# Kernel optimization log

Hardware: AMD Instinct MI355X
Metric: run time of the kernel (lower is better)

## Reference

```python
import jax, jax.numpy as jnp
import numpy as np

HEADS = 4
HID = 64
IN_DIM = 128
N_WIRES, N_TERM, N_ACT = 50, 20, 10
NEG_SLOPE = 0.2


def gat_conv(x, src, dst, ea, W, We, a_src, a_dst, a_edge, bias, concat):
    """PyG GATConv with edge features, add_self_loops=True, fill_value='mean'."""
    N = x.shape[0]
    H, F = a_src.shape
    # --- add self loops; self-loop edge_attr = mean of incoming edge_attr ---
    deg = jax.ops.segment_sum(jnp.ones((ea.shape[0],), x.dtype), dst, num_segments=N)
    loop_attr = jax.ops.segment_sum(ea, dst, num_segments=N) / jnp.maximum(deg, 1.0)[:, None]
    ar = jnp.arange(N)
    src = jnp.concatenate([src, ar])
    dst = jnp.concatenate([dst, ar])
    ea = jnp.concatenate([ea, loop_attr], axis=0)
    # --- linear transforms ---
    h = (x @ W).reshape(N, H, F)                      # [N,H,F]
    a_s = jnp.einsum('nhf,hf->nh', h, a_src)          # [N,H]
    a_d = jnp.einsum('nhf,hf->nh', h, a_dst)
    he = (ea @ We).reshape(-1, H, F)                  # [E2,H,F]
    a_e = jnp.einsum('ehf,hf->eh', he, a_edge)        # [E2,H]
    # --- attention logits + softmax over edges grouped by destination ---
    alpha = jax.nn.leaky_relu(a_s[src] + a_d[dst] + a_e, negative_slope=NEG_SLOPE)
    amax = jax.ops.segment_max(alpha, dst, num_segments=N)
    ex = jnp.exp(alpha - amax[dst])
    denom = jax.ops.segment_sum(ex, dst, num_segments=N)
    alpha = ex / (denom[dst] + 1e-16)                 # [E2,H]
    # --- message passing: gather src feats, weight, scatter-sum to dst ---
    out = jax.ops.segment_sum(h[src] * alpha[..., None], dst, num_segments=N)  # [N,H,F]
    out = out.reshape(N, H * F) if concat else out.mean(axis=1)
    return out + bias


def setup_inputs() -> dict:
    key = jax.random.key(0)
    ks = jax.random.split(key, 24)
    N, E = 20000, 320000
    x = jax.random.normal(ks[0], (N, IN_DIM), jnp.float32)
    edge_index = jax.random.randint(ks[1], (2, E), 0, N, dtype=jnp.int64)
    edge_attr = jax.random.normal(ks[2], (E, 2), jnp.float32)
    s = 0.1
    p = {
        'W1': jax.random.normal(ks[3], (IN_DIM, HEADS * HID)) * s,
        'We1': jax.random.normal(ks[4], (2, HEADS * HID)) * s,
        'as1': jax.random.normal(ks[5], (HEADS, HID)) * s,
        'ad1': jax.random.normal(ks[6], (HEADS, HID)) * s,
        'ae1': jax.random.normal(ks[7], (HEADS, HID)) * s,
        'b1': jnp.zeros((HEADS * HID,), jnp.float32),
        'W2': jax.random.normal(ks[8], (HEADS * HID, HEADS * HID)) * s,
        'We2': jax.random.normal(ks[9], (2, HEADS * HID)) * s,
        'as2': jax.random.normal(ks[10], (HEADS, HID)) * s,
        'ad2': jax.random.normal(ks[11], (HEADS, HID)) * s,
        'ae2': jax.random.normal(ks[12], (HEADS, HID)) * s,
        'b2': jnp.zeros((HID,), jnp.float32),
        'Ww': jax.random.normal(ks[13], (HID, N_WIRES)) * s,
        'bw': jnp.zeros((N_WIRES,), jnp.float32),
        'Wt': jax.random.normal(ks[14], (HID, N_TERM)) * s,
        'bt': jnp.zeros((N_TERM,), jnp.float32),
        'Wa': jax.random.normal(ks[15], (HID, N_ACT)) * s,
        'ba': jnp.zeros((N_ACT,), jnp.float32),
    }
    return {'x': x, 'edge_index': edge_index, 'edge_attr': edge_attr, **p}


def reference(x, edge_index, edge_attr, W1, We1, as1, ad1, ae1, b1,
              W2, We2, as2, ad2, ae2, b2, Ww, bw, Wt, bt, Wa, ba):
    src, dst = edge_index[0], edge_index[1]
    h = jax.nn.elu(gat_conv(x, src, dst, edge_attr, W1, We1, as1, ad1, ae1, b1, True))
    h = jax.nn.elu(gat_conv(h, src, dst, edge_attr, W2, We2, as2, ad2, ae2, b2, False))
    wire_logits = h @ Ww + bw
    terminal_logits = h @ Wt + bt
    action_logits = h @ Wa + ba
    return (wire_logits, terminal_logits, action_logits)
```

## Files before the change

### kernel.cpp

```cpp
#include <hip/hip_runtime.h>
#include <math.h>

#define N_NODES 20000
#define N_EDGES 320000
#define D1      256
#define WCAP    128
#define NSCAT   1250

typedef __attribute__((ext_vector_type(8))) short    bf16x8;
typedef __attribute__((ext_vector_type(4))) float    f32x4;
typedef __attribute__((ext_vector_type(8))) unsigned short u16x8;

__device__ inline float wred_sum(float v) {
#pragma unroll
  for (int o = 32; o > 0; o >>= 1) v += __shfl_xor(v, o, 64);
  return v;
}

__device__ inline unsigned short f2b(float v) {
  unsigned u = __float_as_uint(v);
  unsigned r = (u + 0x7fffu + ((u >> 16) & 1u)) >> 16;
  return (unsigned short)r;
}
__device__ inline float b2f(unsigned short h) {
  return __uint_as_float(((unsigned)h) << 16);
}

__global__ __launch_bounds__(256) void k_prep(
    const int* __restrict__ ei, const float* __restrict__ ea,
    int* __restrict__ deg, int* __restrict__ src_slot, float* __restrict__ ea_slot,
    const float* __restrict__ W1, unsigned short* __restrict__ WT1h,
    unsigned short* __restrict__ WT1l,
    const float* __restrict__ W2, unsigned short* __restrict__ WT2h,
    unsigned short* __restrict__ WT2l,
    const float* __restrict__ We1, const float* __restrict__ ae1,
    const float* __restrict__ We2, const float* __restrict__ ae2,
    float* __restrict__ qb,
    const float* __restrict__ Ww, const float* __restrict__ Wt,
    const float* __restrict__ Wa,
    const float* __restrict__ bw, const float* __restrict__ bt,
    const float* __restrict__ ba,
    unsigned short* __restrict__ WallTh, unsigned short* __restrict__ WallTl,
    float* __restrict__ biasAll) {
  int bid = blockIdx.x, t = threadIdx.x;
  if (bid < NSCAT) {
    int e = bid * 256 + t;
    int s = ei[e], d = ei[N_EDGES + e];
    float2 e2 = *(const float2*)&ea[e * 2];
    int pos = atomicAdd(&deg[d], 1);
    if (pos < WCAP) {
      int slot = d * WCAP + pos;
      src_slot[slot] = s;
      *(float2*)&ea_slot[(size_t)slot * 2] = e2;
    }
  } else if (bid < NSCAT + 128) {
    int i = (bid - NSCAT) * 256 + t;
    int k = i >> 8, n = i & 255;
    float v = W1[i];
    unsigned short h = f2b(v);
    WT1h[n * 128 + k] = h;
    WT1l[n * 128 + k] = f2b(v - b2f(h));
  } else if (bid < NSCAT + 384) {
    int i = (bid - NSCAT - 128) * 256 + t;
    int k = i >> 8, n = i & 255;
    float v = W2[i];
    unsigned short h = f2b(v);
    WT2h[n * 256 + k] = h;
    WT2l[n * 256 + k] = f2b(v - b2f(h));
  } else if (bid == NSCAT + 384) {
    int lane = t & 63, w = t >> 6;
    const float* We = (w >> 1) ? We2 : We1;
    const float* ae = (w >> 1) ? ae2 : ae1;
    int c = w & 1;
#pragma unroll
    for (int h = 0; h < 4; h++) {
      float p = We[c * D1 + h * 64 + lane] * ae[h * 64 + lane];
      p = wred_sum(p);
      if (lane == 0) qb[(w >> 1) * 8 + c * 4 + h] = p;
    }
    if (t < 80) biasAll[t] = (t < 50) ? bw[t] : (t < 70) ? bt[t - 50] : ba[t - 70];
  } else {
    int i = (bid - NSCAT - 385) * 256 + t;
    int j = i >> 6, f = i & 63;
    float v = 0.f;
    if (j < 50)      v = Ww[f * 50 + j];
    else if (j < 70) v = Wt[f * 20 + (j - 50)];
    else if (j < 80) v = Wa[f * 10 + (j - 70)];
    unsigned short h = f2b(v);
    WallTh[j * 64 + f] = h;
    WallTl[j * 64 + f] = f2b(v - b2f(h));
  }
}

#define LDK 40
template <bool AF32>
__global__ __launch_bounds__(256) void k_gemm_mfma(
    const float* __restrict__ Af, const unsigned short* __restrict__ Ah,
    const unsigned short* __restrict__ BTh, const unsigned short* __restrict__ BTl,
    unsigned short* __restrict__ Chi,
    const float* __restrict__ asw, const float* __restrict__ adw,
    float* __restrict__ asb, float* __restrict__ adb,
    int M, int K) {
  __shared__ unsigned short sAh[128 * LDK];
  __shared__ unsigned short sBh[128 * LDK], sBl[128 * LDK];
  int tid = threadIdx.x;
  int lane = tid & 63, wid = tid >> 6;
  int wr = wid >> 1, wc = wid & 1;
  int row0 = blockIdx.y * 128, col0 = blockIdx.x * 128;
  int aRow = wr * 64, bRow = wc * 64;

  f32x4 acc[4][4];
#pragma unroll
  for (int i = 0; i < 4; i++)
#pragma unroll
    for (int j = 0; j < 4; j++) acc[i][j] = (f32x4){0.f, 0.f, 0.f, 0.f};

  int c0i = tid * 2;
  int r0 = c0i >> 2, ko0 = (c0i & 3) * 8;
  int c1i = tid * 2 + 1;
  int r1 = c1i >> 2, ko1 = (c1i & 3) * 8;

  int q8 = (lane >> 4) * 8;
  int rsel = lane & 15;

  const u16x8 z8 = {0, 0, 0, 0, 0, 0, 0, 0};
  int ga0 = row0 + r0, ga1 = row0 + r1;
  bool va0 = ga0 < M, va1 = ga1 < M;
  size_t arow0 = (size_t)ga0 * K, arow1 = (size_t)ga1 * K;
  size_t brow0 = (size_t)(col0 + r0) * K, brow1 = (size_t)(col0 + r1) * K;

  auto ldA = [&](size_t rowoff, bool valid, int kk) -> u16x8 {
    if (!valid) return z8;
    if constexpr (AF32) {
      float4 f0 = *(const float4*)&Af[rowoff + kk];
      float4 f1 = *(const float4*)&Af[rowoff + kk + 4];
      u16x8 r;
      r[0] = f2b(f0.x); r[1] = f2b(f0.y); r[2] = f2b(f0.z); r[3] = f2b(f0.w);
      r[4] = f2b(f1.x); r[5] = f2b(f1.y); r[6] = f2b(f1.z); r[7] = f2b(f1.w);
      return r;
    } else {
      return *(const u16x8*)&Ah[rowoff + kk];
    }
  };

  u16x8 ca0 = ldA(arow0, va0, ko0), ca1 = ldA(arow1, va1, ko1);
  u16x8 cbh0 = *(const u16x8*)&BTh[brow0 + ko0];
  u16x8 cbl0 = *(const u16x8*)&BTl[brow0 + ko0];
  u16x8 cbh1 = *(const u16x8*)&BTh[brow1 + ko1];
  u16x8 cbl1 = *(const u16x8*)&BTl[brow1 + ko1];

  for (int k0 = 0; k0 < K; k0 += 32) {
    *(u16x8*)&sAh[r0 * LDK + ko0] = ca0;
    *(u16x8*)&sAh[r1 * LDK + ko1] = ca1;
    *(u16x8*)&sBh[r0 * LDK + ko0] = cbh0;
    *(u16x8*)&sBl[r0 * LDK + ko0] = cbl0;
    *(u16x8*)&sBh[r1 * LDK + ko1] = cbh1;
    *(u16x8*)&sBl[r1 * LDK + ko1] = cbl1;
    __syncthreads();

    if (k0 + 32 < K) {
      int kn = k0 + 32;
      ca0 = ldA(arow0, va0, kn + ko0);
      ca1 = ldA(arow1, va1, kn + ko1);
      cbh0 = *(const u16x8*)&BTh[brow0 + kn + ko0];
      cbl0 = *(const u16x8*)&BTl[brow0 + kn + ko0];
      cbh1 = *(const u16x8*)&BTh[brow1 + kn + ko1];
      cbl1 = *(const u16x8*)&BTl[brow1 + kn + ko1];
    }

    bf16x8 fah[4], fbh[4], fbl[4];
#pragma unroll
    for (int i = 0; i < 4; i++) {
      int ar = aRow + i * 16 + rsel;
      int br = bRow + i * 16 + rsel;
      fah[i] = *(const bf16x8*)&sAh[ar * LDK + q8];
      fbh[i] = *(const bf16x8*)&sBh[br * LDK + q8];
      fbl[i] = *(const bf16x8*)&sBl[br * LDK + q8];
    }
#pragma unroll
    for (int i = 0; i < 4; i++)
#pragma unroll
      for (int j = 0; j < 4; j++) {
        acc[i][j] = __builtin_amdgcn_mfma_f32_16x16x32_bf16(fah[i], fbh[j], acc[i][j], 0, 0, 0);
        acc[i][j] = __builtin_amdgcn_mfma_f32_16x16x32_bf16(fah[i], fbl[j], acc[i][j], 0, 0, 0);
      }
    __syncthreads();
  }

  int rq = (lane >> 4) * 4;
  int head = (col0 + bRow) >> 6;
  float sa[4], sd[4];
#pragma unroll
  for (int j = 0; j < 4; j++) {
    sa[j] = asw[head * 64 + j * 16 + rsel];
    sd[j] = adw[head * 64 + j * 16 + rsel];
  }
#pragma unroll
  for (int i = 0; i < 4; i++) {
#pragma unroll
    for (int j = 0; j < 4; j++) {
      int gcol = col0 + bRow + j * 16 + rsel;
#pragma unroll
      for (int r = 0; r < 4; r++) {
        int grow = row0 + aRow + i * 16 + rq + r;
        if (grow < M) Chi[(size_t)grow * D1 + gcol] = f2b(acc[i][j][r]);
      }
    }
#pragma unroll
    for (int r = 0; r < 4; r++) {
      float ps = 0.f, pd = 0.f;
#pragma unroll
      for (int j = 0; j < 4; j++) {
        ps = fmaf(acc[i][j][r], sa[j], ps);
        pd = fmaf(acc[i][j][r], sd[j], pd);
      }
#pragma unroll
      for (int o = 1; o < 16; o <<= 1) {
        ps += __shfl_xor(ps, o, 64);
        pd += __shfl_xor(pd, o, 64);
      }
      int grow = row0 + aRow + i * 16 + rq + r;
      if ((lane & 15) == 0 && grow < M) {
        asb[grow * 4 + head] = ps;
        adb[grow * 4 + head] = pd;
      }
    }
  }
}

__global__ __launch_bounds__(256) void k_heads_mfma(
    const unsigned short* __restrict__ Ah, const unsigned short* __restrict__ Al,
    const unsigned short* __restrict__ BTh, const unsigned short* __restrict__ BTl,
    const float* __restrict__ biasAll, float* __restrict__ out, int M) {
  __shared__ unsigned short sAh[128 * LDK], sAl[128 * LDK];
  __shared__ unsigned short sBh[128 * LDK], sBl[128 * LDK];
  const int K = 64;
  int tid = threadIdx.x;
  int lane = tid & 63, wid = tid >> 6;
  int wr = wid >> 1, wc = wid & 1;
  int row0 = blockIdx.x * 128;
  int aRow = wr * 64, bRow = wc * 64;

  f32x4 acc[4][4];
#pragma unroll
  for (int i = 0; i < 4; i++)
#pragma unroll
    for (int j = 0; j < 4; j++) acc[i][j] = (f32x4){0.f, 0.f, 0.f, 0.f};

  int c0i = tid * 2;
  int r0 = c0i >> 2, ko0 = (c0i & 3) * 8;
  int c1i = tid * 2 + 1;
  int r1 = c1i >> 2, ko1 = (c1i & 3) * 8;
  int q8 = (lane >> 4) * 8;
  int rsel = lane & 15;

  for (int k0 = 0; k0 < K; k0 += 32) {
    u16x8 z = {0, 0, 0, 0, 0, 0, 0, 0};
    int ga0 = row0 + r0, ga1 = row0 + r1;
    u16x8 vah0 = (ga0 < M) ? *(const u16x8*)&Ah[(size_t)ga0 * K + k0 + ko0] : z;
    u16x8 val0 = (ga0 < M) ? *(const u16x8*)&Al[(size_t)ga0 * K + k0 + ko0] : z;
    u16x8 vah1 = (ga1 < M) ? *(const u16x8*)&Ah[(size_t)ga1 * K + k0 + ko1] : z;
    u16x8 val1 = (ga1 < M) ? *(const u16x8*)&Al[(size_t)ga1 * K + k0 + ko1] : z;
    u16x8 vbh0 = *(const u16x8*)&BTh[(size_t)r0 * K + k0 + ko0];
    u16x8 vbl0 = *(const u16x8*)&BTl[(size_t)r0 * K + k0 + ko0];
    u16x8 vbh1 = *(const u16x8*)&BTh[(size_t)r1 * K + k0 + ko1];
    u16x8 vbl1 = *(const u16x8*)&BTl[(size_t)r1 * K + k0 + ko1];
    *(u16x8*)&sAh[r0 * LDK + ko0] = vah0;
    *(u16x8*)&sAl[r0 * LDK + ko0] = val0;
    *(u16x8*)&sAh[r1 * LDK + ko1] = vah1;
    *(u16x8*)&sAl[r1 * LDK + ko1] = val1;
    *(u16x8*)&sBh[r0 * LDK + ko0] = vbh0;
    *(u16x8*)&sBl[r0 * LDK + ko0] = vbl0;
    *(u16x8*)&sBh[r1 * LDK + ko1] = vbh1;
    *(u16x8*)&sBl[r1 * LDK + ko1] = vbl1;
    __syncthreads();

    bf16x8 fah[4], fal[4], fbh[4], fbl[4];
#pragma unroll
    for (int i = 0; i < 4; i++) {
      int ar = aRow + i * 16 + rsel;
      int br = bRow + i * 16 + rsel;
      fah[i] = *(const bf16x8*)&sAh[ar * LDK + q8];
      fal[i] = *(const bf16x8*)&sAl[ar * LDK + q8];
      fbh[i] = *(const bf16x8*)&sBh[br * LDK + q8];
      fbl[i] = *(const bf16x8*)&sBl[br * LDK + q8];
    }
#pragma unroll
    for (int i = 0; i < 4; i++)
#pragma unroll
      for (int j = 0; j < 4; j++) {
        acc[i][j] = __builtin_amdgcn_mfma_f32_16x16x32_bf16(fah[i], fbh[j], acc[i][j], 0, 0, 0);
        acc[i][j] = __builtin_amdgcn_mfma_f32_16x16x32_bf16(fah[i], fbl[j], acc[i][j], 0, 0, 0);
        acc[i][j] = __builtin_amdgcn_mfma_f32_16x16x32_bf16(fal[i], fbh[j], acc[i][j], 0, 0, 0);
      }
    __syncthreads();
  }

  int rq = (lane >> 4) * 4;
#pragma unroll
  for (int j = 0; j < 4; j++) {
    int gcol = bRow + j * 16 + rsel;
    if (gcol < 80) {
      float bj = biasAll[gcol];
      float* op; int cols, jj;
      if (gcol < 50)      { op = out;                 cols = 50; jj = gcol; }
      else if (gcol < 70) { op = out + N_NODES * 50;  cols = 20; jj = gcol - 50; }
      else                { op = out + N_NODES * 70;  cols = 10; jj = gcol - 70; }
#pragma unroll
      for (int i = 0; i < 4; i++) {
#pragma unroll
        for (int r = 0; r < 4; r++) {
          int grow = row0 + aRow + i * 16 + rq + r;
          if (grow < M) op[(size_t)grow * cols + jj] = acc[i][j][r] + bj;
        }
      }
    }
  }
}

template <bool CONCAT>
__global__ __launch_bounds__(256) void k_aggregate(
    const unsigned short* __restrict__ feath,
    const int* __restrict__ deg_arr,
    const int* __restrict__ src_slot, const float* __restrict__ ea_slot,
    const float* __restrict__ asb, const float* __restrict__ adb,
    const float* __restrict__ q, const float* __restrict__ bias,
    unsigned short* __restrict__ outh,
    unsigned short* __restrict__ outf_h, unsigned short* __restrict__ outf_l) {
  __shared__ float slog[4][4][WCAP];
  __shared__ int   ssrc[4][WCAP];
  int t = threadIdx.x, lane = t & 63, w = t >> 6;
  int n = blockIdx.x * 4 + w;
  int deg = min(deg_arr[n], WCAP);
  int b = n * WCAP;

  float4 qv0 = *(const float4*)q;
  float4 qv1 = *(const float4*)(q + 4);
  float4 ad4 = *(const float4*)&adb[(size_t)n * 4];
  float4 asn = *(const float4*)&asb[(size_t)n * 4];

  int degR = (deg + 15) & ~15;
  if (degR == 0) degR = 16;
  int   sreg[2] = {n, n};
  float e0r[2] = {0.f, 0.f}, e1r[2] = {0.f, 0.f};
#pragma unroll
  for (int p = 0; p < 2; p++) {
    int j = lane + p * 64;
    if (j < degR) {
      int s = n; float e0v = 0.f, e1v = 0.f;
      if (j < deg) {
        s = src_slot[b + j];
        float2 ee = *(const float2*)&ea_slot[(size_t)(b + j) * 2];
        e0v = ee.x; e1v = ee.y;
      }
      ssrc[w][j] = s;
      sreg[p] = s; e0r[p] = e0v; e1r[p] = e1v;
    }
  }
  int es = lane >> 5, cg = lane & 31, hh = cg >> 3;
  const unsigned short* fb = feath + cg * 8;
  u16x8 pf[8];
#pragma unroll
  for (int q8 = 0; q8 < 8; q8++) {
    int s = __shfl(sreg[0], 2 * q8 + es, 64);
    pf[q8] = *(const u16x8*)&fb[(size_t)s * D1];
  }
  float lv[2][4];
#pragma unroll
  for (int p = 0; p < 2; p++) {
    int j = lane + p * 64;
    float l0 = -1e30f, l1 = -1e30f, l2 = -1e30f, l3 = -1e30f;
    if (j < deg) {
      float4 as4 = *(const float4*)&asb[(size_t)sreg[p] * 4];
      float e0v = e0r[p], e1v = e1r[p];
      l0 = as4.x + ad4.x + e0v * qv0.x + e1v * qv1.x; l0 = (l0 > 0.f) ? l0 : 0.2f * l0;
      l1 = as4.y + ad4.y + e0v * qv0.y + e1v * qv1.y; l1 = (l1 > 0.f) ? l1 : 0.2f * l1;
      l2 = as4.z + ad4.z + e0v * qv0.z + e1v * qv1.z; l2 = (l2 > 0.f) ? l2 : 0.2f * l2;
      l3 = as4.w + ad4.w + e0v * qv0.w + e1v * qv1.w; l3 = (l3 > 0.f) ? l3 : 0.2f * l3;
    }
    lv[p][0] = l0; lv[p][1] = l1; lv[p][2] = l2; lv[p][3] = l3;
  }
  float dinv = 1.f / fmaxf((float)deg, 1.f);
  float e0m = wred_sum(e0r[0] + e0r[1]) * dinv;
  float e1m = wred_sum(e1r[0] + e1r[1]) * dinv;
  float ls[4];
  ls[0] = asn.x + ad4.x + e0m * qv0.x + e1m * qv1.x;
  ls[1] = asn.y + ad4.y + e0m * qv0.y + e1m * qv1.y;
  ls[2] = asn.z + ad4.z + e0m * qv0.z + e1m * qv1.z;
  ls[3] = asn.w + ad4.w + e0m * qv0.w + e1m * qv1.w;
#pragma unroll
  for (int h = 0; h < 4; h++) ls[h] = (ls[h] > 0.f) ? ls[h] : 0.2f * ls[h];
  float ex[2][4];
#pragma unroll
  for (int p = 0; p < 2; p++)
#pragma unroll
    for (int h = 0; h < 4; h++) ex[p][h] = __expf(lv[p][h]);
  float inv[4], wself[4];
#pragma unroll
  for (int h = 0; h < 4; h++) {
    float eself = __expf(ls[h]);
    float ss = wred_sum(ex[0][h] + ex[1][h]) + eself;
    inv[h] = 1.f / (ss + 1e-16f);
    wself[h] = eself * inv[h];
  }
#pragma unroll
  for (int p = 0; p < 2; p++) {
    int j = lane + p * 64;
    if (j < degR) {
#pragma unroll
      for (int h = 0; h < 4; h++) slog[w][h][j] = ex[p][h] * inv[h];
    }
  }
  float acc8[8] = {};
#pragma unroll
  for (int q8 = 0; q8 < 8; q8++) {
    float ww = slog[w][hh][2 * q8 + es];
#pragma unroll
    for (int k = 0; k < 8; k++) acc8[k] = fmaf(ww, b2f((unsigned short)pf[q8][k]), acc8[k]);
  }
  for (int j0 = 16; j0 < degR; j0 += 16) {
    u16x8 f[8];
#pragma unroll
    for (int q8 = 0; q8 < 8; q8++)
      f[q8] = *(const u16x8*)&fb[(size_t)ssrc[w][j0 + 2 * q8 + es] * D1];
#pragma unroll
    for (int q8 = 0; q8 < 8; q8++) {
      float ww = slog[w][hh][j0 + 2 * q8 + es];
#pragma unroll
      for (int k = 0; k < 8; k++) acc8[k] = fmaf(ww, b2f((unsigned short)f[q8][k]), acc8[k]);
    }
  }
  if (es == 0) {
    u16x8 fs = *(const u16x8*)&fb[(size_t)n * D1];
    float ws2 = wself[hh];
#pragma unroll
    for (int k = 0; k < 8; k++) acc8[k] = fmaf(ws2, b2f((unsigned short)fs[k]), acc8[k]);
  }
#pragma unroll
  for (int k = 0; k < 8; k++) acc8[k] += __shfl_xor(acc8[k], 32, 64);
  if (CONCAT) {
    if (es == 0) {
      u16x8 hi8;
#pragma unroll
      for (int k = 0; k < 8; k++) {
        float v2 = acc8[k] + bias[cg * 8 + k];
        v2 = (v2 > 0.f) ? v2 : (__expf(v2) - 1.f);
        hi8[k] = f2b(v2);
      }
      *(u16x8*)&outh[(size_t)n * D1 + cg * 8] = hi8;
    }
  } else {
#pragma unroll
    for (int k = 0; k < 8; k++) {
      acc8[k] += __shfl_xor(acc8[k], 8, 64);
      acc8[k] += __shfl_xor(acc8[k], 16, 64);
    }
    if (es == 0 && cg < 8) {
      u16x8 hi8, lo8;
#pragma unroll
      for (int k = 0; k < 8; k++) {
        float v2 = acc8[k] * 0.25f + bias[cg * 8 + k];
        v2 = (v2 > 0.f) ? v2 : (__expf(v2) - 1.f);
        unsigned short hh2 = f2b(v2);
        hi8[k] = hh2;
        lo8[k] = f2b(v2 - b2f(hh2));
      }
      *(u16x8*)&outf_h[(size_t)n * 64 + cg * 8] = hi8;
      *(u16x8*)&outf_l[(size_t)n * 64 + cg * 8] = lo8;
    }
  }
}

extern "C" void kernel_launch(void* const* d_in, const int* in_sizes, int n_in,
                              void* d_out, int out_size, void* d_ws, size_t ws_size,
                              hipStream_t stream) {
  const float* x   = (const float*)d_in[0];
  const int*   ei  = (const int*)d_in[1];
  const float* ea  = (const float*)d_in[2];
  const float* W1  = (const float*)d_in[3];
  const float* We1 = (const float*)d_in[4];
  const float* as1 = (const float*)d_in[5];
  const float* ad1 = (const float*)d_in[6];
  const float* ae1 = (const float*)d_in[7];
  const float* b1  = (const float*)d_in[8];
  const float* W2  = (const float*)d_in[9];
  const float* We2 = (const float*)d_in[10];
  const float* as2 = (const float*)d_in[11];
  const float* ad2 = (const float*)d_in[12];
  const float* ae2 = (const float*)d_in[13];
  const float* b2  = (const float*)d_in[14];
  const float* Ww  = (const float*)d_in[15];
  const float* bw  = (const float*)d_in[16];
  const float* Wt  = (const float*)d_in[17];
  const float* bt  = (const float*)d_in[18];
  const float* Wa  = (const float*)d_in[19];
  const float* ba  = (const float*)d_in[20];
  float* out = (float*)d_out;

  char* ws = (char*)d_ws;
  size_t off = 0;
  auto alloc = [&](size_t bytes) {
    void* p = ws + off;
    off += (bytes + 255) & ~(size_t)255;
    return p;
  };
  unsigned short* Ah     = (unsigned short*)alloc((size_t)N_NODES * D1 * 2);
  unsigned short* Bfh    = (unsigned short*)alloc((size_t)N_NODES * D1 * 2);
  unsigned short* h2h    = (unsigned short*)alloc((size_t)N_NODES * 64 * 2);
  unsigned short* h2l    = (unsigned short*)alloc((size_t)N_NODES * 64 * 2);
  unsigned short* WT1h   = (unsigned short*)alloc((size_t)128 * 256 * 2);
  unsigned short* WT1l   = (unsigned short*)alloc((size_t)128 * 256 * 2);
  unsigned short* WT2h   = (unsigned short*)alloc((size_t)256 * 256 * 2);
  unsigned short* WT2l   = (unsigned short*)alloc((size_t)256 * 256 * 2);
  unsigned short* WallTh = (unsigned short*)alloc((size_t)128 * 64 * 2);
  unsigned short* WallTl = (unsigned short*)alloc((size_t)128 * 64 * 2);
  float*          biasAll= (float*)alloc(80 * 4);
  int*   src_slot = (int*)alloc((size_t)N_NODES * WCAP * 4);
  float* ea_slot  = (float*)alloc((size_t)N_NODES * WCAP * 2 * 4);
  int*   deg      = (int*)alloc((size_t)N_NODES * 4);
  float* asb      = (float*)alloc((size_t)N_NODES * 4 * 4);
  float* adb      = (float*)alloc((size_t)N_NODES * 4 * 4);
  float* qb       = (float*)alloc(64);

  hipMemsetAsync(deg, 0, (size_t)N_NODES * 4, stream);

  k_prep<<<NSCAT + 385 + 32, 256, 0, stream>>>(
      ei, ea, deg, src_slot, ea_slot,
      W1, WT1h, WT1l, W2, WT2h, WT2l, We1, ae1, We2, ae2, qb,
      Ww, Wt, Wa, bw, bt, ba, WallTh, WallTl, biasAll);

  dim3 ggemm(2, (N_NODES + 127) / 128);

  k_gemm_mfma<true><<<ggemm, 256, 0, stream>>>(x, nullptr, WT1h, WT1l, Ah,
                                               as1, ad1, asb, adb, N_NODES, 128);
  k_aggregate<true><<<N_NODES / 4, 256, 0, stream>>>(
      Ah, deg, src_slot, ea_slot, asb, adb, qb, b1, Bfh, nullptr, nullptr);

  k_gemm_mfma<false><<<ggemm, 256, 0, stream>>>(nullptr, Bfh, WT2h, WT2l, Ah,
                                                as2, ad2, asb, adb, N_NODES, 256);
  k_aggregate<false><<<N_NODES / 4, 256, 0, stream>>>(
      Ah, deg, src_slot, ea_slot, asb, adb, qb + 8, b2, nullptr, h2h, h2l);

  k_heads_mfma<<<(N_NODES + 127) / 128, 256, 0, stream>>>(
      h2h, h2l, WallTh, WallTl, biasAll, out, N_NODES);
}
```

Baseline: 230.1 us.

## Fuse output head projections into second GAT aggregation kernel

Result: slower. 282.3 us (+22.7%).

```diff
diff --git a/kernel.cpp b/kernel.cpp
--- a/kernel.cpp
+++ b/kernel.cpp
@@ -6,6 +6,7 @@
 #define D1      256
 #define WCAP    128
 #define NSCAT   1250
+#define NPREP   (NSCAT + 385)
 
 typedef __attribute__((ext_vector_type(8))) short    bf16x8;
 typedef __attribute__((ext_vector_type(4))) float    f32x4;
@@ -35,13 +36,7 @@
     unsigned short* __restrict__ WT2l,
     const float* __restrict__ We1, const float* __restrict__ ae1,
     const float* __restrict__ We2, const float* __restrict__ ae2,
-    float* __restrict__ qb,
-    const float* __restrict__ Ww, const float* __restrict__ Wt,
-    const float* __restrict__ Wa,
-    const float* __restrict__ bw, const float* __restrict__ bt,
-    const float* __restrict__ ba,
-    unsigned short* __restrict__ WallTh, unsigned short* __restrict__ WallTl,
-    float* __restrict__ biasAll) {
+    float* __restrict__ qb) {
   int bid = blockIdx.x, t = threadIdx.x;
   if (bid < NSCAT) {
     int e = bid * 256 + t;
@@ -67,7 +62,7 @@
     unsigned short h = f2b(v);
     WT2h[n * 256 + k] = h;
     WT2l[n * 256 + k] = f2b(v - b2f(h));
-  } else if (bid == NSCAT + 384) {
+  } else {
     int lane = t & 63, w = t >> 6;
     const float* We = (w >> 1) ? We2 : We1;
     const float* ae = (w >> 1) ? ae2 : ae1;
@@ -78,17 +73,6 @@
       p = wred_sum(p);
       if (lane == 0) qb[(w >> 1) * 8 + c * 4 + h] = p;
     }
-    if (t < 80) biasAll[t] = (t < 50) ? bw[t] : (t < 70) ? bt[t - 50] : ba[t - 70];
-  } else {
-    int i = (bid - NSCAT - 385) * 256 + t;
-    int j = i >> 6, f = i & 63;
-    float v = 0.f;
-    if (j < 50)      v = Ww[f * 50 + j];
-    else if (j < 70) v = Wt[f * 20 + (j - 50)];
-    else if (j < 80) v = Wa[f * 10 + (j - 70)];
-    unsigned short h = f2b(v);
-    WallTh[j * 64 + f] = h;
-    WallTl[j * 64 + f] = f2b(v - b2f(h));
   }
 }
 
@@ -119,7 +103,6 @@
   int r0 = c0i >> 2, ko0 = (c0i & 3) * 8;
   int c1i = tid * 2 + 1;
   int r1 = c1i >> 2, ko1 = (c1i & 3) * 8;
-
   int q8 = (lane >> 4) * 8;
   int rsel = lane & 15;
 
@@ -228,96 +211,6 @@
   }
 }
 
-__global__ __launch_bounds__(256) void k_heads_mfma(
-    const unsigned short* __restrict__ Ah, const unsigned short* __restrict__ Al,
-    const unsigned short* __restrict__ BTh, const unsigned short* __restrict__ BTl,
-    const float* __restrict__ biasAll, float* __restrict__ out, int M) {
-  __shared__ unsigned short sAh[128 * LDK], sAl[128 * LDK];
-  __shared__ unsigned short sBh[128 * LDK], sBl[128 * LDK];
-  const int K = 64;
-  int tid = threadIdx.x;
-  int lane = tid & 63, wid = tid >> 6;
-  int wr = wid >> 1, wc = wid & 1;
-  int row0 = blockIdx.x * 128;
-  int aRow = wr * 64, bRow = wc * 64;
-
-  f32x4 acc[4][4];
-#pragma unroll
-  for (int i = 0; i < 4; i++)
-#pragma unroll
-    for (int j = 0; j < 4; j++) acc[i][j] = (f32x4){0.f, 0.f, 0.f, 0.f};
-
-  int c0i = tid * 2;
-  int r0 = c0i >> 2, ko0 = (c0i & 3) * 8;
-  int c1i = tid * 2 + 1;
-  int r1 = c1i >> 2, ko1 = (c1i & 3) * 8;
-  int q8 = (lane >> 4) * 8;
-  int rsel = lane & 15;
-
-  for (int k0 = 0; k0 < K; k0 += 32) {
-    u16x8 z = {0, 0, 0, 0, 0, 0, 0, 0};
-    int ga0 = row0 + r0, ga1 = row0 + r1;
-    u16x8 vah0 = (ga0 < M) ? *(const u16x8*)&Ah[(size_t)ga0 * K + k0 + ko0] : z;
-    u16x8 val0 = (ga0 < M) ? *(const u16x8*)&Al[(size_t)ga0 * K + k0 + ko0] : z;
-    u16x8 vah1 = (ga1 < M) ? *(const u16x8*)&Ah[(size_t)ga1 * K + k0 + ko1] : z;
-    u16x8 val1 = (ga1 < M) ? *(const u16x8*)&Al[(size_t)ga1 * K + k0 + ko1] : z;
-    u16x8 vbh0 = *(const u16x8*)&BTh[(size_t)r0 * K + k0 + ko0];
-    u16x8 vbl0 = *(const u16x8*)&BTl[(size_t)r0 * K + k0 + ko0];
-    u16x8 vbh1 = *(const u16x8*)&BTh[(size_t)r1 * K + k0 + ko1];
-    u16x8 vbl1 = *(const u16x8*)&BTl[(size_t)r1 * K + k0 + ko1];
-    *(u16x8*)&sAh[r0 * LDK + ko0] = vah0;
-    *(u16x8*)&sAl[r0 * LDK + ko0] = val0;
-    *(u16x8*)&sAh[r1 * LDK + ko1] = vah1;
-    *(u16x8*)&sAl[r1 * LDK + ko1] = val1;
-    *(u16x8*)&sBh[r0 * LDK + ko0] = vbh0;
-    *(u16x8*)&sBl[r0 * LDK + ko0] = vbl0;
-    *(u16x8*)&sBh[r1 * LDK + ko1] = vbh1;
-    *(u16x8*)&sBl[r1 * LDK + ko1] = vbl1;
-    __syncthreads();
-
-    bf16x8 fah[4], fal[4], fbh[4], fbl[4];
-#pragma unroll
-    for (int i = 0; i < 4; i++) {
-      int ar = aRow + i * 16 + rsel;
-      int br = bRow + i * 16 + rsel;
-      fah[i] = *(const bf16x8*)&sAh[ar * LDK + q8];
-      fal[i] = *(const bf16x8*)&sAl[ar * LDK + q8];
-      fbh[i] = *(const bf16x8*)&sBh[br * LDK + q8];
-      fbl[i] = *(const bf16x8*)&sBl[br * LDK + q8];
-    }
-#pragma unroll
-    for (int i = 0; i < 4; i++)
-#pragma unroll
-      for (int j = 0; j < 4; j++) {
-        acc[i][j] = __builtin_amdgcn_mfma_f32_16x16x32_bf16(fah[i], fbh[j], acc[i][j], 0, 0, 0);
-        acc[i][j] = __builtin_amdgcn_mfma_f32_16x16x32_bf16(fah[i], fbl[j], acc[i][j], 0, 0, 0);
-        acc[i][j] = __builtin_amdgcn_mfma_f32_16x16x32_bf16(fal[i], fbh[j], acc[i][j], 0, 0, 0);
-      }
-    __syncthreads();
-  }
-
-  int rq = (lane >> 4) * 4;
-#pragma unroll
-  for (int j = 0; j < 4; j++) {
-    int gcol = bRow + j * 16 + rsel;
-    if (gcol < 80) {
-      float bj = biasAll[gcol];
-      float* op; int cols, jj;
-      if (gcol < 50)      { op = out;                 cols = 50; jj = gcol; }
-      else if (gcol < 70) { op = out + N_NODES * 50;  cols = 20; jj = gcol - 50; }
-      else                { op = out + N_NODES * 70;  cols = 10; jj = gcol - 70; }
-#pragma unroll
-      for (int i = 0; i < 4; i++) {
-#pragma unroll
-        for (int r = 0; r < 4; r++) {
-          int grow = row0 + aRow + i * 16 + rq + r;
-          if (grow < M) op[(size_t)grow * cols + jj] = acc[i][j][r] + bj;
-        }
-      }
-    }
-  }
-}
-
 template <bool CONCAT>
 __global__ __launch_bounds__(256) void k_aggregate(
     const unsigned short* __restrict__ feath,
@@ -326,7 +219,10 @@
     const float* __restrict__ asb, const float* __restrict__ adb,
     const float* __restrict__ q, const float* __restrict__ bias,
     unsigned short* __restrict__ outh,
-    unsigned short* __restrict__ outf_h, unsigned short* __restrict__ outf_l) {
+    const float* __restrict__ Ww, const float* __restrict__ Wt,
+    const float* __restrict__ Wa,
+    const float* __restrict__ bw, const float* __restrict__ bt,
+    const float* __restrict__ ba, float* __restrict__ out) {
   __shared__ float slog[4][4][WCAP];
   __shared__ int   ssrc[4][WCAP];
   int t = threadIdx.x, lane = t & 63, w = t >> 6;
@@ -438,7 +334,7 @@
   }
 #pragma unroll
   for (int k = 0; k < 8; k++) acc8[k] += __shfl_xor(acc8[k], 32, 64);
-  if (CONCAT) {
+  if constexpr (CONCAT) {
     if (es == 0) {
       u16x8 hi8;
 #pragma unroll
@@ -450,23 +346,60 @@
       *(u16x8*)&outh[(size_t)n * D1 + cg * 8] = hi8;
     }
   } else {
+    __shared__ float sW[80 * 64];
+    __shared__ float sh2[4][64];
 #pragma unroll
     for (int k = 0; k < 8; k++) {
       acc8[k] += __shfl_xor(acc8[k], 8, 64);
       acc8[k] += __shfl_xor(acc8[k], 16, 64);
     }
     if (es == 0 && cg < 8) {
-      u16x8 hi8, lo8;
+      float vv[8];
 #pragma unroll
       for (int k = 0; k < 8; k++) {
         float v2 = acc8[k] * 0.25f + bias[cg * 8 + k];
-        v2 = (v2 > 0.f) ? v2 : (__expf(v2) - 1.f);
-        unsigned short hh2 = f2b(v2);
-        hi8[k] = hh2;
-        lo8[k] = f2b(v2 - b2f(hh2));
-      }
-      *(u16x8*)&outf_h[(size_t)n * 64 + cg * 8] = hi8;
-      *(u16x8*)&outf_l[(size_t)n * 64 + cg * 8] = lo8;
+        vv[k] = (v2 > 0.f) ? v2 : (__expf(v2) - 1.f);
+      }
+      *(float4*)&sh2[w][cg * 8]     = (float4){vv[0], vv[1], vv[2], vv[3]};
+      *(float4*)&sh2[w][cg * 8 + 4] = (float4){vv[4], vv[5], vv[6], vv[7]};
+    }
+    for (int i = t; i < 80 * 64; i += 256) {
+      int j = i >> 6, f = i & 63;
+      sW[i] = (j < 50) ? Ww[f * 50 + j]
+            : (j < 70) ? Wt[f * 20 + (j - 50)]
+                       : Wa[f * 10 + (j - 70)];
+    }
+    __syncthreads();
+    const float* h2w = sh2[w];
+    {
+      int j = lane;
+      float a = 0.f;
+#pragma unroll
+      for (int f = 0; f < 64; f += 4) {
+        float4 hv = *(const float4*)&h2w[f];
+        float4 wv = *(const float4*)&sW[j * 64 + f];
+        a = fmaf(hv.x, wv.x, a); a = fmaf(hv.y, wv.y, a);
+        a = fmaf(hv.z, wv.z, a); a = fmaf(hv.w, wv.w, a);
+      }
+      float* op; int cols, jj; float bj;
+      if (j < 50)      { op = out;                cols = 50; jj = j;      bj = bw[j];      }
+      else             { op = out + N_NODES * 50; cols = 20; jj = j - 50; bj = bt[j - 50]; }
+      op[(size_t)n * cols + jj] = a + bj;
+    }
+    if (lane < 16) {
+      int j = 64 + lane;
+      float a = 0.f;
+#pragma unroll
+      for (int f = 0; f < 64; f += 4) {
+        float4 hv = *(const float4*)&h2w[f];
+        float4 wv = *(const float4*)&sW[j * 64 + f];
+        a = fmaf(hv.x, wv.x, a); a = fmaf(hv.y, wv.y, a);
+        a = fmaf(hv.z, wv.z, a); a = fmaf(hv.w, wv.w, a);
+      }
+      float* op; int cols, jj; float bj;
+      if (j < 70)      { op = out + N_NODES * 50; cols = 20; jj = j - 50; bj = bt[j - 50]; }
+      else             { op = out + N_NODES * 70; cols = 10; jj = j - 70; bj = ba[j - 70]; }
+      op[(size_t)n * cols + jj] = a + bj;
     }
   }
 }
@@ -506,15 +439,10 @@
   };
   unsigned short* Ah     = (unsigned short*)alloc((size_t)N_NODES * D1 * 2);
   unsigned short* Bfh    = (unsigned short*)alloc((size_t)N_NODES * D1 * 2);
-  unsigned short* h2h    = (unsigned short*)alloc((size_t)N_NODES * 64 * 2);
-  unsigned short* h2l    = (unsigned short*)alloc((size_t)N_NODES * 64 * 2);
   unsigned short* WT1h   = (unsigned short*)alloc((size_t)128 * 256 * 2);
   unsigned short* WT1l   = (unsigned short*)alloc((size_t)128 * 256 * 2);
   unsigned short* WT2h   = (unsigned short*)alloc((size_t)256 * 256 * 2);
   unsigned short* WT2l   = (unsigned short*)alloc((size_t)256 * 256 * 2);
-  unsigned short* WallTh = (unsigned short*)alloc((size_t)128 * 64 * 2);
-  unsigned short* WallTl = (unsigned short*)alloc((size_t)128 * 64 * 2);
-  float*          biasAll= (float*)alloc(80 * 4);
   int*   src_slot = (int*)alloc((size_t)N_NODES * WCAP * 4);
   float* ea_slot  = (float*)alloc((size_t)N_NODES * WCAP * 2 * 4);
   int*   deg      = (int*)alloc((size_t)N_NODES * 4);
@@ -524,23 +452,21 @@
 
   hipMemsetAsync(deg, 0, (size_t)N_NODES * 4, stream);
 
-  k_prep<<<NSCAT + 385 + 32, 256, 0, stream>>>(
+  k_prep<<<NPREP, 256, 0, stream>>>(
       ei, ea, deg, src_slot, ea_slot,
-      W1, WT1h, WT1l, W2, WT2h, WT2l, We1, ae1, We2, ae2, qb,
-      Ww, Wt, Wa, bw, bt, ba, WallTh, WallTl, biasAll);
+      W1, WT1h, WT1l, W2, WT2h, WT2l, We1, ae1, We2, ae2, qb);
 
   dim3 ggemm(2, (N_NODES + 127) / 128);
 
   k_gemm_mfma<true><<<ggemm, 256, 0, stream>>>(x, nullptr, WT1h, WT1l, Ah,
                                                as1, ad1, asb, adb, N_NODES, 128);
   k_aggregate<true><<<N_NODES / 4, 256, 0, stream>>>(
-      Ah, deg, src_slot, ea_slot, asb, adb, qb, b1, Bfh, nullptr, nullptr);
+      Ah, deg, src_slot, ea_slot, asb, adb, qb, b1, Bfh,
+      nullptr, nullptr, nullptr, nullptr, nullptr, nullptr, nullptr);
 
   k_gemm_mfma<false><<<ggemm, 256, 0, stream>>>(nullptr, Bfh, WT2h, WT2l, Ah,
                                                 as2, ad2, asb, adb, N_NODES, 256);
   k_aggregate<false><<<N_NODES / 4, 256, 0, stream>>>(
-      Ah, deg, src_slot, ea_slot, asb, adb, qb + 8, b2, nullptr, h2h, h2l);
-
-  k_heads_mfma<<<(N_NODES + 127) / 128, 256, 0, stream>>>(
-      h2h, h2l, WallTh, WallTl, biasAll, out, N_NODES);
-}
+      Ah, deg, src_slot, ea_slot, asb, adb, qb + 8, b2, nullptr,
+      Ww, Wt, Wa, bw, bt, ba, out);
+}
```
